# Performance work log

Measured on AMD Instinct MI355X. Metric: run time of the kernel, lower is better.

The kernel has to match this reference:

```python
import jax, jax.numpy as jnp
import numpy as np

N = 262144      # samples
D_EMB = 512     # embedding dim
C = 1024        # number of compounds
D_DOSE = 8      # number of dose ranks
MARGIN = 0.1


def setup_inputs() -> dict:
    key = jax.random.key(0)
    k_emb, k_comp, k_dose = jax.random.split(key, 3)
    embeddings = jax.random.normal(k_emb, (N, D_EMB), dtype=jnp.float32)
    compound_labels = jax.random.randint(k_comp, (N,), 0, C, dtype=jnp.int32)
    dose_labels = jax.random.randint(k_dose, (N,), 0, D_DOSE, dtype=jnp.int32)
    return {"embeddings": embeddings, "compound_labels": compound_labels, "dose_labels": dose_labels}


def reference(embeddings, compound_labels, dose_labels):
    # origin = F.normalize(mean(embeddings, dim=0, keepdim=True), dim=-1)
    mu = embeddings.mean(axis=0, keepdims=True)                      # [1, d]
    norm = jnp.maximum(jnp.linalg.norm(mu, axis=-1, keepdims=True), 1e-12)
    origin = mu / norm                                               # [1, d]
    dist = 1.0 - jnp.sum(embeddings * origin, axis=-1)               # [N]

    # fused segment-mean over (compound, dose) grid
    seg = compound_labels.astype(jnp.int32) * D_DOSE + dose_labels.astype(jnp.int32)
    num_seg = C * D_DOSE
    seg_sum = jax.ops.segment_sum(dist, seg, num_segments=num_seg)
    seg_cnt = jax.ops.segment_sum(jnp.ones_like(dist), seg, num_segments=num_seg)
    seg_mean = (seg_sum / jnp.maximum(seg_cnt, 1.0)).reshape(C, D_DOSE)
    present = (seg_cnt > 0).reshape(C, D_DOSE)

    # adjacent present-dose pairs within each compound: sweep dose axis (small, fixed D_DOSE)
    # tracking the last present dose's mean per compound -> same pairs as torch's
    # unique().sort() adjacency over doses actually present.
    last_mean = jnp.zeros((C,), dtype=dist.dtype)
    last_valid = jnp.zeros((C,), dtype=bool)
    loss = jnp.asarray(0.0, dtype=dist.dtype)
    count = jnp.asarray(0.0, dtype=dist.dtype)
    for d in range(D_DOSE):
        cur = seg_mean[:, d]
        pres = present[:, d]
        valid = pres & last_valid
        viol = jnp.maximum(MARGIN - (cur - last_mean), 0.0)          # relu(margin - (d_high - d_low))
        loss = loss + jnp.sum(jnp.where(valid, viol, 0.0))
        count = count + jnp.sum(valid.astype(dist.dtype))
        last_mean = jnp.where(pres, cur, last_mean)
        last_valid = last_valid | pres

    return jnp.where(count > 0, loss / jnp.maximum(count, 1.0), 0.0)
```

## Files before the change

kernel.cpp:

```cpp
#include <hip/hip_runtime.h>
#include <hip/hip_bf16.h>

#define D_EMB    512
#define D4       128
#define NCOMP    1024
#define NDOSE    8
#define NSEG     (NCOMP * NDOSE)
#define MARGIN_F 0.1f

typedef unsigned int uint32;

__global__ __launch_bounds__(256) void hist_kernel(
    const int* __restrict__ comp, const int* __restrict__ dose,
    uint32* __restrict__ hist, int n)
{
    __shared__ uint32 lh[NSEG];
    for (int i = threadIdx.x; i < NSEG; i += blockDim.x) lh[i] = 0;
    __syncthreads();
    const int stride = gridDim.x * blockDim.x;
    for (int r = blockIdx.x * blockDim.x + threadIdx.x; r < n; r += stride) {
        const int s = comp[r] * NDOSE + dose[r];
        atomicAdd(&lh[s], 1u);
    }
    __syncthreads();
    for (int i = threadIdx.x; i < NSEG; i += blockDim.x) {
        const uint32 v = lh[i];
        if (v) atomicAdd(&hist[i], v);
    }
}

__global__ __launch_bounds__(1024) void scan_kernel(
    const uint32* __restrict__ hist, uint32* __restrict__ off,
    uint32* __restrict__ cur)
{
    const int t = threadIdx.x;
    uint32 v[8];
    uint32 tot = 0;
    #pragma unroll
    for (int j = 0; j < 8; ++j) { v[j] = hist[t * 8 + j]; tot += v[j]; }

    __shared__ uint32 sums[1024];
    sums[t] = tot;
    __syncthreads();
    for (int o = 1; o < 1024; o <<= 1) {
        uint32 add = (t >= o) ? sums[t - o] : 0u;
        __syncthreads();
        sums[t] += add;
        __syncthreads();
    }
    uint32 run = sums[t] - tot;
    #pragma unroll
    for (int j = 0; j < 8; ++j) {
        off[t * 8 + j] = run;
        cur[t * 8 + j] = run;
        run += v[j];
    }
}

__global__ __launch_bounds__(256) void scatter_kernel(
    const int* __restrict__ comp, const int* __restrict__ dose,
    uint32* __restrict__ cur, uint32* __restrict__ perm, int n)
{
    const int stride = gridDim.x * blockDim.x;
    for (int r = blockIdx.x * blockDim.x + threadIdx.x; r < n; r += stride) {
        const int s = comp[r] * NDOSE + dose[r];
        const uint32 pos = atomicAdd(&cur[s], 1u);
        perm[pos] = (uint32)r;
    }
}

#define PERM_LDS 128
__global__ __launch_bounds__(256) void segsum_kernel(
    const float* __restrict__ emb, const uint32* __restrict__ off,
    const uint32* __restrict__ hist, const uint32* __restrict__ perm,
    float* __restrict__ S)
{
    const int s    = blockIdx.x;
    const int c4   = threadIdx.x & 127;
    const int rsub = threadIdx.x >> 7;
    const uint32 beg = off[s];
    const uint32 cnt = hist[s];
    const float4* __restrict__ E = (const float4*)emb;

    __shared__ uint32 lperm[PERM_LDS];
    const uint32 staged = (cnt < (uint32)PERM_LDS) ? cnt : (uint32)PERM_LDS;
    for (uint32 i = threadIdx.x; i < staged; i += blockDim.x)
        lperm[i] = perm[beg + i];
    __syncthreads();

    float4 acc = make_float4(0.f, 0.f, 0.f, 0.f);
    uint32 i = (uint32)rsub;
    for (; i < staged; i += 2) {
        const uint32 r = lperm[i];
        const float4 v = E[(size_t)r * D4 + c4];
        acc.x += v.x; acc.y += v.y; acc.z += v.z; acc.w += v.w;
    }
    for (; i < cnt; i += 2) {
        const uint32 r = perm[beg + i];
        const float4 v = E[(size_t)r * D4 + c4];
        acc.x += v.x; acc.y += v.y; acc.z += v.z; acc.w += v.w;
    }

    __shared__ float4 part[256];
    part[threadIdx.x] = acc;
    __syncthreads();
    if (threadIdx.x < 128) {
        const float4 a = part[threadIdx.x];
        const float4 b = part[threadIdx.x + 128];
        float4 o;
        o.x = a.x + b.x; o.y = a.y + b.y; o.z = a.z + b.z; o.w = a.w + b.w;
        ((float4*)S)[(size_t)s * D4 + c4] = o;
    }
}

__global__ __launch_bounds__(128) void musum_kernel(
    const float* __restrict__ S, float* __restrict__ mu_sum)
{
    const int c4 = threadIdx.x;
    const float4* __restrict__ S4 = (const float4*)S;
    float4 acc = make_float4(0.f, 0.f, 0.f, 0.f);
    for (int s = blockIdx.x; s < NSEG; s += gridDim.x) {
        const float4 v = S4[(size_t)s * D4 + c4];
        acc.x += v.x; acc.y += v.y; acc.z += v.z; acc.w += v.w;
    }
    const int c = c4 * 4;
    atomicAdd(&mu_sum[c + 0], acc.x);
    atomicAdd(&mu_sum[c + 1], acc.y);
    atomicAdd(&mu_sum[c + 2], acc.z);
    atomicAdd(&mu_sum[c + 3], acc.w);
}

__global__ __launch_bounds__(256) void dot_kernel(
    const float* __restrict__ S, const float* __restrict__ mu_sum,
    const uint32* __restrict__ hist, float* __restrict__ seg_mean, float inv_n)
{
    const int lane = threadIdx.x & 63;
    const int wave = threadIdx.x >> 6;
    const int wglob = blockIdx.x * (blockDim.x >> 6) + wave;
    const int wtot  = gridDim.x * (blockDim.x >> 6);

    const float4* __restrict__ MU = (const float4*)mu_sum;
    float4 m0 = MU[lane];
    float4 m1 = MU[lane + 64];
    m0.x *= inv_n; m0.y *= inv_n; m0.z *= inv_n; m0.w *= inv_n;
    m1.x *= inv_n; m1.y *= inv_n; m1.z *= inv_n; m1.w *= inv_n;
    float sq = m0.x * m0.x + m0.y * m0.y + m0.z * m0.z + m0.w * m0.w
             + m1.x * m1.x + m1.y * m1.y + m1.z * m1.z + m1.w * m1.w;
    #pragma unroll
    for (int o = 32; o; o >>= 1) sq += __shfl_xor(sq, o, 64);
    const float inv_norm = 1.0f / fmaxf(sqrtf(sq), 1e-12f);
    float4 o0, o1;
    o0.x = m0.x * inv_norm; o0.y = m0.y * inv_norm;
    o0.z = m0.z * inv_norm; o0.w = m0.w * inv_norm;
    o1.x = m1.x * inv_norm; o1.y = m1.y * inv_norm;
    o1.z = m1.z * inv_norm; o1.w = m1.w * inv_norm;

    const float4* __restrict__ S4 = (const float4*)S;
    for (int s = wglob; s < NSEG; s += wtot) {
        const float4 v0 = S4[(size_t)s * D4 + lane];
        const float4 v1 = S4[(size_t)s * D4 + lane + 64];
        float p = v0.x * o0.x + v0.y * o0.y + v0.z * o0.z + v0.w * o0.w
                + v1.x * o1.x + v1.y * o1.y + v1.z * o1.z + v1.w * o1.w;
        #pragma unroll
        for (int o = 32; o; o >>= 1) p += __shfl_xor(p, o, 64);
        if (lane == 0) {
            const float cntf = (float)hist[s];
            seg_mean[s] = (cntf - p) / fmaxf(cntf, 1.f);
        }
    }
}

__global__ __launch_bounds__(1024) void epilogue_kernel(
    const float* __restrict__ seg_mean, const uint32* __restrict__ hist,
    float* __restrict__ out)
{
    const int c = threadIdx.x;
    float loss = 0.f, cntv = 0.f;
    {
        float last_mean = 0.f;
        bool  last_valid = false;
        #pragma unroll
        for (int d = 0; d < NDOSE; ++d) {
            const bool  pres = hist[c * NDOSE + d] > 0u;
            const float mean = seg_mean[c * NDOSE + d];
            if (pres && last_valid) {
                loss += fmaxf(MARGIN_F - (mean - last_mean), 0.f);
                cntv += 1.f;
            }
            if (pres) { last_mean = mean; last_valid = true; }
        }
    }
    __shared__ float sl[1024];
    __shared__ float sc[1024];
    sl[c] = loss; sc[c] = cntv;
    __syncthreads();
    #pragma unroll
    for (int o = 512; o; o >>= 1) {
        if (c < o) { sl[c] += sl[c + o]; sc[c] += sc[c + o]; }
        __syncthreads();
    }
    if (c == 0) out[0] = (sc[0] > 0.f) ? (sl[0] / fmaxf(sc[0], 1.f)) : 0.f;
}

extern "C" void kernel_launch(void* const* d_in, const int* in_sizes, int n_in,
                              void* d_out, int out_size, void* d_ws, size_t ws_size,
                              hipStream_t stream)
{
    const float* emb  = (const float*)d_in[0];
    const int*   comp = (const int*)d_in[1];
    const int*   dose = (const int*)d_in[2];
    float*       out  = (float*)d_out;
    const int n = in_sizes[1];

    uint32* hist    = (uint32*)d_ws;
    float*  mu_sum  = (float*)(hist + NSEG);
    uint32* off     = (uint32*)(mu_sum + D_EMB);
    uint32* cur     = off + NSEG;
    uint32* perm    = cur + NSEG;
    float*  seg_mean= (float*)(perm + n);
    float*  S       = seg_mean + NSEG + D_EMB;

    hipMemsetAsync(d_ws, 0, (size_t)(NSEG + D_EMB) * sizeof(float), stream);

    hist_kernel    <<<256, 256, 0, stream>>>(comp, dose, hist, n);
    scan_kernel    <<<1, 1024, 0, stream>>>(hist, off, cur);
    scatter_kernel <<<1024, 256, 0, stream>>>(comp, dose, cur, perm, n);
    segsum_kernel  <<<NSEG, 256, 0, stream>>>(emb, off, hist, perm, S);
    musum_kernel   <<<128, 128, 0, stream>>>(S, mu_sum);
    dot_kernel     <<<128, 256, 0, stream>>>(S, mu_sum, hist, seg_mean,
                                             1.0f / (float)n);
    epilogue_kernel<<<1, 1024, 0, stream>>>(seg_mean, hist, out);
}
```

Measured before the change: 768.7 us.

## Merge sort and finish stages into cooperative kernels with grid sync

Replaces the memset plus histogram/scan/scatter launches with one cooperative kernel that zeroes buffers, builds the histogram with global atomics, scans in block 0 and scatters, separated by grid.sync. The musum, dot and epilogue kernels are likewise merged into a second cooperative kernel. The aim is to cut per-launch overhead and small-kernel tail latency. In exchange, the histogram drops its shared-memory privatization and uses direct global atomics, and grid syncs add their own cost.

```diff
diff --git a/kernel.cpp b/kernel.cpp
--- a/kernel.cpp
+++ b/kernel.cpp
@@ -1,5 +1,8 @@
 #include <hip/hip_runtime.h>
 #include <hip/hip_bf16.h>
+#include <hip/hip_cooperative_groups.h>
+
+namespace cg = cooperative_groups;
 
 #define D_EMB    512
 #define D4       128
@@ -10,59 +13,50 @@
 
 typedef unsigned int uint32;
 
-__global__ __launch_bounds__(256) void hist_kernel(
+__global__ __launch_bounds__(1024, 4) void sort_coop_kernel(
     const int* __restrict__ comp, const int* __restrict__ dose,
-    uint32* __restrict__ hist, int n)
-{
-    __shared__ uint32 lh[NSEG];
-    for (int i = threadIdx.x; i < NSEG; i += blockDim.x) lh[i] = 0;
-    __syncthreads();
-    const int stride = gridDim.x * blockDim.x;
-    for (int r = blockIdx.x * blockDim.x + threadIdx.x; r < n; r += stride) {
-        const int s = comp[r] * NDOSE + dose[r];
-        atomicAdd(&lh[s], 1u);
-    }
-    __syncthreads();
-    for (int i = threadIdx.x; i < NSEG; i += blockDim.x) {
-        const uint32 v = lh[i];
-        if (v) atomicAdd(&hist[i], v);
-    }
-}
-
-__global__ __launch_bounds__(1024) void scan_kernel(
-    const uint32* __restrict__ hist, uint32* __restrict__ off,
-    uint32* __restrict__ cur)
-{
-    const int t = threadIdx.x;
-    uint32 v[8];
-    uint32 tot = 0;
-    #pragma unroll
-    for (int j = 0; j < 8; ++j) { v[j] = hist[t * 8 + j]; tot += v[j]; }
+    uint32* __restrict__ hist, float* __restrict__ mu_sum,
+    uint32* __restrict__ off, uint32* __restrict__ cur,
+    uint32* __restrict__ perm, int n)
+{
+    cg::grid_group grid = cg::this_grid();
+    const int tid = blockIdx.x * blockDim.x + threadIdx.x;
+    const int nth = gridDim.x * blockDim.x;
+
+    for (int i = tid; i < NSEG; i += nth) hist[i] = 0u;
+    if (tid < D_EMB) mu_sum[tid] = 0.f;
+    grid.sync();
+
+    for (int r = tid; r < n; r += nth)
+        atomicAdd(&hist[comp[r] * NDOSE + dose[r]], 1u);
+    grid.sync();
 
     __shared__ uint32 sums[1024];
-    sums[t] = tot;
-    __syncthreads();
-    for (int o = 1; o < 1024; o <<= 1) {
-        uint32 add = (t >= o) ? sums[t - o] : 0u;
+    if (blockIdx.x == 0) {
+        const int t = threadIdx.x;
+        uint32 v[8];
+        uint32 tot = 0;
+        #pragma unroll
+        for (int j = 0; j < 8; ++j) { v[j] = hist[t * 8 + j]; tot += v[j]; }
+        sums[t] = tot;
         __syncthreads();
-        sums[t] += add;
-        __syncthreads();
-    }
-    uint32 run = sums[t] - tot;
-    #pragma unroll
-    for (int j = 0; j < 8; ++j) {
-        off[t * 8 + j] = run;
-        cur[t * 8 + j] = run;
-        run += v[j];
-    }
-}
-
-__global__ __launch_bounds__(256) void scatter_kernel(
-    const int* __restrict__ comp, const int* __restrict__ dose,
-    uint32* __restrict__ cur, uint32* __restrict__ perm, int n)
-{
-    const int stride = gridDim.x * blockDim.x;
-    for (int r = blockIdx.x * blockDim.x + threadIdx.x; r < n; r += stride) {
+        for (int o = 1; o < 1024; o <<= 1) {
+            uint32 add = (t >= o) ? sums[t - o] : 0u;
+            __syncthreads();
+            sums[t] += add;
+            __syncthreads();
+        }
+        uint32 run = sums[t] - tot;
+        #pragma unroll
+        for (int j = 0; j < 8; ++j) {
+            off[t * 8 + j] = run;
+            cur[t * 8 + j] = run;
+            run += v[j];
+        }
+    }
+    grid.sync();
+
+    for (int r = tid; r < n; r += nth) {
         const int s = comp[r] * NDOSE + dose[r];
         const uint32 pos = atomicAdd(&cur[s], 1u);
         perm[pos] = (uint32)r;
@@ -113,93 +107,105 @@
     }
 }
 
-__global__ __launch_bounds__(128) void musum_kernel(
-    const float* __restrict__ S, float* __restrict__ mu_sum)
-{
-    const int c4 = threadIdx.x;
+__global__ __launch_bounds__(1024, 4) void finish_coop_kernel(
+    const float* __restrict__ S, const uint32* __restrict__ hist,
+    float* __restrict__ mu_sum, float* __restrict__ seg_mean,
+    float* __restrict__ out, float inv_n)
+{
+    cg::grid_group grid = cg::this_grid();
+    __shared__ float4 part4[1024];
     const float4* __restrict__ S4 = (const float4*)S;
-    float4 acc = make_float4(0.f, 0.f, 0.f, 0.f);
-    for (int s = blockIdx.x; s < NSEG; s += gridDim.x) {
-        const float4 v = S4[(size_t)s * D4 + c4];
-        acc.x += v.x; acc.y += v.y; acc.z += v.z; acc.w += v.w;
-    }
-    const int c = c4 * 4;
-    atomicAdd(&mu_sum[c + 0], acc.x);
-    atomicAdd(&mu_sum[c + 1], acc.y);
-    atomicAdd(&mu_sum[c + 2], acc.z);
-    atomicAdd(&mu_sum[c + 3], acc.w);
-}
-
-__global__ __launch_bounds__(256) void dot_kernel(
-    const float* __restrict__ S, const float* __restrict__ mu_sum,
-    const uint32* __restrict__ hist, float* __restrict__ seg_mean, float inv_n)
-{
-    const int lane = threadIdx.x & 63;
-    const int wave = threadIdx.x >> 6;
-    const int wglob = blockIdx.x * (blockDim.x >> 6) + wave;
-    const int wtot  = gridDim.x * (blockDim.x >> 6);
-
-    const float4* __restrict__ MU = (const float4*)mu_sum;
-    float4 m0 = MU[lane];
-    float4 m1 = MU[lane + 64];
-    m0.x *= inv_n; m0.y *= inv_n; m0.z *= inv_n; m0.w *= inv_n;
-    m1.x *= inv_n; m1.y *= inv_n; m1.z *= inv_n; m1.w *= inv_n;
-    float sq = m0.x * m0.x + m0.y * m0.y + m0.z * m0.z + m0.w * m0.w
-             + m1.x * m1.x + m1.y * m1.y + m1.z * m1.z + m1.w * m1.w;
-    #pragma unroll
-    for (int o = 32; o; o >>= 1) sq += __shfl_xor(sq, o, 64);
-    const float inv_norm = 1.0f / fmaxf(sqrtf(sq), 1e-12f);
-    float4 o0, o1;
-    o0.x = m0.x * inv_norm; o0.y = m0.y * inv_norm;
-    o0.z = m0.z * inv_norm; o0.w = m0.w * inv_norm;
-    o1.x = m1.x * inv_norm; o1.y = m1.y * inv_norm;
-    o1.z = m1.z * inv_norm; o1.w = m1.w * inv_norm;
-
-    const float4* __restrict__ S4 = (const float4*)S;
-    for (int s = wglob; s < NSEG; s += wtot) {
-        const float4 v0 = S4[(size_t)s * D4 + lane];
-        const float4 v1 = S4[(size_t)s * D4 + lane + 64];
-        float p = v0.x * o0.x + v0.y * o0.y + v0.z * o0.z + v0.w * o0.w
-                + v1.x * o1.x + v1.y * o1.y + v1.z * o1.z + v1.w * o1.w;
-        #pragma unroll
-        for (int o = 32; o; o >>= 1) p += __shfl_xor(p, o, 64);
-        if (lane == 0) {
-            const float cntf = (float)hist[s];
-            seg_mean[s] = (cntf - p) / fmaxf(cntf, 1.f);
-        }
-    }
-}
-
-__global__ __launch_bounds__(1024) void epilogue_kernel(
-    const float* __restrict__ seg_mean, const uint32* __restrict__ hist,
-    float* __restrict__ out)
-{
-    const int c = threadIdx.x;
-    float loss = 0.f, cntv = 0.f;
-    {
-        float last_mean = 0.f;
-        bool  last_valid = false;
-        #pragma unroll
-        for (int d = 0; d < NDOSE; ++d) {
-            const bool  pres = hist[c * NDOSE + d] > 0u;
-            const float mean = seg_mean[c * NDOSE + d];
-            if (pres && last_valid) {
-                loss += fmaxf(MARGIN_F - (mean - last_mean), 0.f);
-                cntv += 1.f;
+
+    {
+        const int c4  = threadIdx.x & 127;
+        const int sub = threadIdx.x >> 7;
+        float4 acc = make_float4(0.f, 0.f, 0.f, 0.f);
+        for (int s = blockIdx.x * 8 + sub; s < NSEG; s += gridDim.x * 8) {
+            const float4 v = S4[(size_t)s * D4 + c4];
+            acc.x += v.x; acc.y += v.y; acc.z += v.z; acc.w += v.w;
+        }
+        part4[threadIdx.x] = acc;
+        __syncthreads();
+        if (threadIdx.x < 128) {
+            float4 a = part4[threadIdx.x];
+            #pragma unroll
+            for (int sb = 1; sb < 8; ++sb) {
+                const float4 b = part4[threadIdx.x + 128 * sb];
+                a.x += b.x; a.y += b.y; a.z += b.z; a.w += b.w;
             }
-            if (pres) { last_mean = mean; last_valid = true; }
-        }
-    }
-    __shared__ float sl[1024];
-    __shared__ float sc[1024];
-    sl[c] = loss; sc[c] = cntv;
-    __syncthreads();
-    #pragma unroll
-    for (int o = 512; o; o >>= 1) {
-        if (c < o) { sl[c] += sl[c + o]; sc[c] += sc[c + o]; }
+            const int c = threadIdx.x * 4;
+            atomicAdd(&mu_sum[c + 0], a.x);
+            atomicAdd(&mu_sum[c + 1], a.y);
+            atomicAdd(&mu_sum[c + 2], a.z);
+            atomicAdd(&mu_sum[c + 3], a.w);
+        }
+    }
+    grid.sync();
+
+    {
+        const int lane  = threadIdx.x & 63;
+        const int wglob = blockIdx.x * (int)(blockDim.x >> 6) + (threadIdx.x >> 6);
+        const int wtot  = gridDim.x * (int)(blockDim.x >> 6);
+
+        const float4* __restrict__ MU = (const float4*)mu_sum;
+        float4 m0 = MU[lane];
+        float4 m1 = MU[lane + 64];
+        m0.x *= inv_n; m0.y *= inv_n; m0.z *= inv_n; m0.w *= inv_n;
+        m1.x *= inv_n; m1.y *= inv_n; m1.z *= inv_n; m1.w *= inv_n;
+        float sq = m0.x * m0.x + m0.y * m0.y + m0.z * m0.z + m0.w * m0.w
+                 + m1.x * m1.x + m1.y * m1.y + m1.z * m1.z + m1.w * m1.w;
+        #pragma unroll
+        for (int o = 32; o; o >>= 1) sq += __shfl_xor(sq, o, 64);
+        const float inv_norm = 1.0f / fmaxf(sqrtf(sq), 1e-12f);
+        float4 o0, o1;
+        o0.x = m0.x * inv_norm; o0.y = m0.y * inv_norm;
+        o0.z = m0.z * inv_norm; o0.w = m0.w * inv_norm;
+        o1.x = m1.x * inv_norm; o1.y = m1.y * inv_norm;
+        o1.z = m1.z * inv_norm; o1.w = m1.w * inv_norm;
+
+        for (int s = wglob; s < NSEG; s += wtot) {
+            const float4 v0 = S4[(size_t)s * D4 + lane];
+            const float4 v1 = S4[(size_t)s * D4 + lane + 64];
+            float p = v0.x * o0.x + v0.y * o0.y + v0.z * o0.z + v0.w * o0.w
+                    + v1.x * o1.x + v1.y * o1.y + v1.z * o1.z + v1.w * o1.w;
+            #pragma unroll
+            for (int o = 32; o; o >>= 1) p += __shfl_xor(p, o, 64);
+            if (lane == 0) {
+                const float cntf = (float)hist[s];
+                seg_mean[s] = (cntf - p) / fmaxf(cntf, 1.f);
+            }
+        }
+    }
+    grid.sync();
+
+    if (blockIdx.x == 0) {
+        float* sl = (float*)part4;
+        float* sc = sl + 1024;
+        const int c = threadIdx.x;
+        float loss = 0.f, cntv = 0.f;
+        {
+            float last_mean = 0.f;
+            bool  last_valid = false;
+            #pragma unroll
+            for (int d = 0; d < NDOSE; ++d) {
+                const bool  pres = hist[c * NDOSE + d] > 0u;
+                const float mean = seg_mean[c * NDOSE + d];
+                if (pres && last_valid) {
+                    loss += fmaxf(MARGIN_F - (mean - last_mean), 0.f);
+                    cntv += 1.f;
+                }
+                if (pres) { last_mean = mean; last_valid = true; }
+            }
+        }
+        sl[c] = loss; sc[c] = cntv;
         __syncthreads();
-    }
-    if (c == 0) out[0] = (sc[0] > 0.f) ? (sl[0] / fmaxf(sc[0], 1.f)) : 0.f;
+        #pragma unroll
+        for (int o = 512; o; o >>= 1) {
+            if (c < o) { sl[c] += sl[c + o]; sc[c] += sc[c + o]; }
+            __syncthreads();
+        }
+        if (c == 0) out[0] = (sc[0] > 0.f) ? (sl[0] / fmaxf(sc[0], 1.f)) : 0.f;
+    }
 }
 
 extern "C" void kernel_launch(void* const* d_in, const int* in_sizes, int n_in,
@@ -210,7 +216,7 @@
     const int*   comp = (const int*)d_in[1];
     const int*   dose = (const int*)d_in[2];
     float*       out  = (float*)d_out;
-    const int n = in_sizes[1];
+    int n = in_sizes[1];
 
     uint32* hist    = (uint32*)d_ws;
     float*  mu_sum  = (float*)(hist + NSEG);
@@ -220,14 +226,22 @@
     float*  seg_mean= (float*)(perm + n);
     float*  S       = seg_mean + NSEG + D_EMB;
 
-    hipMemsetAsync(d_ws, 0, (size_t)(NSEG + D_EMB) * sizeof(float), stream);
-
-    hist_kernel    <<<256, 256, 0, stream>>>(comp, dose, hist, n);
-    scan_kernel    <<<1, 1024, 0, stream>>>(hist, off, cur);
-    scatter_kernel <<<1024, 256, 0, stream>>>(comp, dose, cur, perm, n);
-    segsum_kernel  <<<NSEG, 256, 0, stream>>>(emb, off, hist, perm, S);
-    musum_kernel   <<<128, 128, 0, stream>>>(S, mu_sum);
-    dot_kernel     <<<128, 256, 0, stream>>>(S, mu_sum, hist, seg_mean,
-                                             1.0f / (float)n);
-    epilogue_kernel<<<1, 1024, 0, stream>>>(seg_mean, hist, out);
-}
+    float inv_n = 1.0f / (float)n;
+
+    {
+        void* argsA[] = { (void*)&comp, (void*)&dose, (void*)&hist,
+                          (void*)&mu_sum, (void*)&off, (void*)&cur,
+                          (void*)&perm, (void*)&n };
+        hipLaunchCooperativeKernel((const void*)sort_coop_kernel,
+                                   dim3(256), dim3(1024), argsA, 0, stream);
+    }
+
+    segsum_kernel<<<NSEG, 256, 0, stream>>>(emb, off, hist, perm, S);
+
+    {
+        void* argsB[] = { (void*)&S, (void*)&hist, (void*)&mu_sum,
+                          (void*)&seg_mean, (void*)&out, (void*)&inv_n };
+        hipLaunchCooperativeKernel((const void*)finish_coop_kernel,
+                                   dim3(256), dim3(1024), argsB, 0, stream);
+    }
+}
```

New measurement: 876.4 us. 1.14x slower.
